# Performance work log

Hardware: AMD Instinct MI355X
Metric: run time of the kernel (lower is better)

The kernel has to match this reference:

```python
import jax, jax.numpy as jnp
import numpy as np

B, N, C, H = 8, 1024, 768, 12
D = C // H  # 64


def setup_inputs() -> dict:
    key = jax.random.key(0)
    ks = jax.random.split(key, 6)
    x = jax.random.normal(ks[0], (B, N, C), dtype=jnp.float32)
    pad_mask = jnp.ones((B, N), dtype=jnp.int32)
    # params (torch Linear stored transposed; here kept as (in, out) for x @ W)
    s = 1.0 / np.sqrt(C)
    w_attn = jax.random.uniform(ks[1], (C, 3 * C), jnp.float32, -s, s)
    b_attn = jax.random.uniform(ks[2], (3 * C,), jnp.float32, -s, s)
    w_proj = jax.random.uniform(ks[3], (C, C), jnp.float32, -s, s)
    b_proj = jax.random.uniform(ks[4], (C,), jnp.float32, -s, s)
    return {"x": x, "pad_mask": pad_mask, "w_attn": w_attn,
            "b_attn": b_attn, "w_proj": w_proj, "b_proj": b_proj}


def reference(x, pad_mask, w_attn, b_attn, w_proj, b_proj):
    # qkv projection
    qkv = x @ w_attn + b_attn                      # [B,N,3C]
    q, k, v = jnp.split(qkv, 3, axis=-1)
    q = q.reshape(B, N, H, D).transpose(0, 2, 1, 3)  # [B,H,N,D]
    k = k.reshape(B, N, H, D).transpose(0, 2, 1, 3)
    v = v.reshape(B, N, H, D).transpose(0, 2, 1, 3)
    scale = 1.0 / np.sqrt(D)
    att = jnp.einsum('bhqd,bhkd->bhqk', q, k) * scale  # [B,H,N,N]
    # NOTE: original code's causal masked_fill is non-in-place and discarded,
    # so the causal mask is NOT applied. Only the pad mask (over query rows) is.
    pm = pad_mask.reshape(B, 1, N, 1)
    att = jnp.where(pm == 0, -jnp.inf, att)
    att = jax.nn.softmax(att, axis=-1)
    out = jnp.einsum('bhqk,bhkd->bhqd', att, v)     # [B,H,N,D]
    out = out.transpose(0, 2, 1, 3).reshape(B, N, C)
    # dropout layers are identity in eval mode
    return out @ w_proj + b_proj
```

## Files before the change

### kernel.cpp

```cpp
#include <hip/hip_runtime.h>
#include <hip/hip_bf16.h>

#define B_  8
#define N_  1024
#define C_  768
#define H_  12
#define D_  64
#define C3  2304
#define C2  1536

typedef unsigned short ushort_t;
typedef __attribute__((ext_vector_type(8))) short bf16x8;
typedef __attribute__((ext_vector_type(4))) float f32x4;
typedef __attribute__((ext_vector_type(4))) unsigned int u32x4;
typedef __attribute__((ext_vector_type(2))) unsigned int u32x2;

__device__ __forceinline__ ushort_t f2bf(float f) {
    union { float f; unsigned int i; } v;
    v.f = f;
    unsigned int x = v.i;
    if ((x & 0x7f800000u) == 0x7f800000u && (x & 0x007fffffu))
        return (ushort_t)((x >> 16) | 0x0040u);
    return (ushort_t)((x + 0x7fffu + ((x >> 16) & 1u)) >> 16);
}

__device__ __forceinline__ void st1(float* p, float v) { *p = v; }
__device__ __forceinline__ void st1(ushort_t* p, float v) { *p = f2bf(v); }

#define NCVT 6144
#define NTA  1728
#define NTP  576

__device__ __forceinline__ void transpose_tile(
    const float* __restrict__ W, ushort_t* __restrict__ WT,
    int K, int Nn, int n0, int k0, float (*t)[33], int tid)
{
    const int tx = tid & 31, ty = tid >> 5;
    #pragma unroll
    for (int i = 0; i < 4; ++i) {
        const int k = ty + i * 8;
        t[k][tx] = W[(size_t)(k0 + k) * Nn + n0 + tx];
    }
    __syncthreads();
    #pragma unroll
    for (int i = 0; i < 4; ++i) {
        const int n = ty + i * 8;
        WT[(size_t)(n0 + n) * K + k0 + tx] = f2bf(t[tx][n]);
    }
}

__global__ __launch_bounds__(256) void prep(
    const float* __restrict__ X, ushort_t* __restrict__ Y,
    const float* __restrict__ Wa, ushort_t* __restrict__ WaT,
    const float* __restrict__ Wp, ushort_t* __restrict__ WpT)
{
    __shared__ float t[32][33];
    const int bid = blockIdx.x;
    const int tid = threadIdx.x;
    if (bid < NCVT) {
        const int i = (bid * 256 + tid) * 4;
        float4 f = *reinterpret_cast<const float4*>(X + i);
        ushort4 o;
        o.x = f2bf(f.x); o.y = f2bf(f.y); o.z = f2bf(f.z); o.w = f2bf(f.w);
        *reinterpret_cast<ushort4*>(Y + i) = o;
    } else if (bid < NCVT + NTA) {
        const int tt = bid - NCVT;
        transpose_tile(Wa, WaT, C_, C3, (tt % (C3 / 32)) * 32,
                       (tt / (C3 / 32)) * 32, t, tid);
    } else {
        const int tt = bid - NCVT - NTA;
        transpose_tile(Wp, WpT, C_, C_, (tt % (C_ / 32)) * 32,
                       (tt / (C_ / 32)) * 32, t, tid);
    }
}

#define GBK 64

__device__ __forceinline__ void gld_lds16(const ushort_t* g, ushort_t* lds) {
    __builtin_amdgcn_global_load_lds(
        (const __attribute__((address_space(1))) void*)g,
        (__attribute__((address_space(3))) void*)lds, 16, 0, 0);
}

template<typename TO, bool SCALEQ>
__global__ __launch_bounds__(256) void gemm_mfma(
    const ushort_t* __restrict__ A, const ushort_t* __restrict__ BT,
    const float* __restrict__ bias, TO* __restrict__ Y, int ldY,
    ushort_t* __restrict__ vtOut, int M, int K, int Nn)
{
    __shared__ ushort_t As[128 * GBK];
    __shared__ ushort_t Bs[128 * GBK];

    const int tid  = threadIdx.x;
    const int wave = tid >> 6;
    const int lane = tid & 63;

    const int nbx  = Nn / 128;
    const int nblk = nbx * (M / 128);
    const int hwid = blockIdx.y * gridDim.x + blockIdx.x;
    const int wid  = (hwid & 7) * (nblk >> 3) + (hwid >> 3);
    const int row0 = (wid / nbx) * 128;
    const int col0 = (wid % nbx) * 128;

    const int wr   = (wave >> 1) * 64;
    const int wc   = (wave & 1) * 64;
    const int l15  = lane & 15;
    const int quad = lane >> 4;
    const int l7   = l15 & 7;

    const int srow = lane >> 3;
    const int sg   = (lane & 7) ^ srow;

    f32x4 acc[4][4] = {};

    for (int k0 = 0; k0 < K; k0 += GBK) {
        __syncthreads();
        #pragma unroll
        for (int it = 0; it < 4; ++it) {
            const int baseRow = wave * 32 + it * 8;
            const int r = baseRow + srow;
            gld_lds16(&A [(size_t)(row0 + r) * K + k0 + sg * 8], &As[baseRow * GBK]);
            gld_lds16(&BT[(size_t)(col0 + r) * K + k0 + sg * 8], &Bs[baseRow * GBK]);
        }
        __syncthreads();

        #pragma unroll
        for (int kc = 0; kc < 2; ++kc) {
            bf16x8 af[4], bf[4];
            #pragma unroll
            for (int i = 0; i < 4; ++i) {
                const int aslot = (kc * 4 + quad) ^ l7;
                af[i] = *reinterpret_cast<const bf16x8*>(
                    &As[(wr + i * 16 + l15) * GBK + aslot * 8]);
                bf[i] = *reinterpret_cast<const bf16x8*>(
                    &Bs[(wc + i * 16 + l15) * GBK + aslot * 8]);
            }
            #pragma unroll
            for (int i = 0; i < 4; ++i)
                #pragma unroll
                for (int j = 0; j < 4; ++j)
                    acc[i][j] = __builtin_amdgcn_mfma_f32_16x16x32_bf16(
                        af[i], bf[j], acc[i][j], 0, 0, 0);
        }
    }

    const float qs = (SCALEQ && (col0 + wc) < C_) ? 0.1803368801f : 1.0f;

    if (vtOut != nullptr && col0 >= C2) {
        #pragma unroll
        for (int i = 0; i < 4; ++i) {
            const int r0 = row0 + wr + i * 16 + quad * 4;
            const int bb = r0 >> 10;
            const int n  = r0 & 1023;
            #pragma unroll
            for (int j = 0; j < 4; ++j) {
                const int c  = col0 + wc + j * 16 + l15;
                const int cv = c - C2;
                const int hh = cv >> 6, d = cv & 63;
                const float bv = bias[c];
                ushort4 o;
                o.x = f2bf(acc[i][j][0] + bv);
                o.y = f2bf(acc[i][j][1] + bv);
                o.z = f2bf(acc[i][j][2] + bv);
                o.w = f2bf(acc[i][j][3] + bv);
                *reinterpret_cast<ushort4*>(
                    &vtOut[((size_t)(bb * H_ + hh) * D_ + d) * N_ + n]) = o;
            }
        }
    } else {
        #pragma unroll
        for (int i = 0; i < 4; ++i) {
            const int r = row0 + wr + i * 16 + quad * 4;
            #pragma unroll
            for (int j = 0; j < 4; ++j) {
                const int c = col0 + wc + j * 16 + l15;
                const float bv = bias[c];
                #pragma unroll
                for (int t = 0; t < 4; ++t)
                    st1(&Y[(size_t)(r + t) * ldY + c], (acc[i][j][t] + bv) * qs);
            }
        }
    }
}

__global__ __launch_bounds__(256) void attn_mfma(
    const ushort_t* __restrict__ qk, const ushort_t* __restrict__ vt,
    const int* __restrict__ pad_mask, ushort_t* __restrict__ y)
{
    __shared__ __align__(16) ushort_t KV[2 * 64 * 64];
    ushort_t* const Ks  = KV;
    ushort_t* const Vts = KV + 64 * 64;

    const int tid  = threadIdx.x;
    const int wave = tid >> 6;
    const int lane = tid & 63;
    const int l15  = lane & 15;
    const int quad = lane >> 4;
    const int l7   = l15 & 7;

    const int wid = (blockIdx.x & 7) * 96 + (blockIdx.x >> 3);
    const int qt = wid & 7;
    const int hb = wid >> 3;
    const int h  = hb % H_;
    const int b  = hb / H_;
    const int q0 = qt * 128 + wave * 32;

    const ushort_t* qkB = qk + (size_t)b * N_ * C2;
    const ushort_t* vtB = vt + ((size_t)(b * H_ + h)) * D_ * N_;
    const int ho = h * D_;

    bf16x8 qf[2][2];
    #pragma unroll
    for (int rt = 0; rt < 2; ++rt)
        #pragma unroll
        for (int kc = 0; kc < 2; ++kc)
            qf[rt][kc] = *reinterpret_cast<const bf16x8*>(
                &qkB[(size_t)(q0 + rt * 16 + l15) * C2 + ho + kc * 32 + quad * 8]);

    int mrow[2][4];
    #pragma unroll
    for (int rt = 0; rt < 2; ++rt)
        #pragma unroll
        for (int t = 0; t < 4; ++t)
            mrow[rt][t] = pad_mask[b * N_ + q0 + rt * 16 + quad * 4 + t];

    f32x4 oacc[2][4] = {};
    float den[2] = {};

    const int srow = lane >> 3;
    const int sg   = (lane & 7) ^ srow;

    for (int k0 = 0; k0 < N_; k0 += 64) {
        __syncthreads();
        #pragma unroll
        for (int it = 0; it < 2; ++it) {
            const int base = wave * 16 + it * 8;
            const int r = base + srow;
            gld_lds16(&qkB[(size_t)(k0 + r) * C2 + C_ + ho + sg * 8],
                      &Ks[base * 64]);
            gld_lds16(&vtB[(size_t)r * N_ + k0 + sg * 8],
                      &Vts[base * 64]);
        }
        __syncthreads();

        f32x4 s[2][4] = {};
        #pragma unroll
        for (int kc = 0; kc < 2; ++kc) {
            bf16x8 kf[4];
            #pragma unroll
            for (int ct = 0; ct < 4; ++ct) {
                const int slot = (kc * 4 + quad) ^ l7;
                kf[ct] = *reinterpret_cast<const bf16x8*>(
                    &Ks[(ct * 16 + l15) * 64 + slot * 8]);
            }
            __builtin_amdgcn_s_setprio(1);
            #pragma unroll
            for (int rt = 0; rt < 2; ++rt)
                #pragma unroll
                for (int ct = 0; ct < 4; ++ct)
                    s[rt][ct] = __builtin_amdgcn_mfma_f32_16x16x32_bf16(
                        kf[ct], qf[rt][kc], s[rt][ct], 0, 0, 0);
            __builtin_amdgcn_s_setprio(0);
        }

        unsigned pk[2][4][2];
        #pragma unroll
        for (int rt = 0; rt < 2; ++rt)
            #pragma unroll
            for (int ct = 0; ct < 4; ++ct) {
                const unsigned x0 = __float_as_uint(
                    __builtin_amdgcn_exp2f(s[rt][ct][0])) + 0x8000u;
                const unsigned x1 = __float_as_uint(
                    __builtin_amdgcn_exp2f(s[rt][ct][1])) + 0x8000u;
                const unsigned x2 = __float_as_uint(
                    __builtin_amdgcn_exp2f(s[rt][ct][2])) + 0x8000u;
                const unsigned x3 = __float_as_uint(
                    __builtin_amdgcn_exp2f(s[rt][ct][3])) + 0x8000u;
                const unsigned c0 = (x0 >> 16) | (x1 & 0xffff0000u);
                const unsigned c1 = (x2 >> 16) | (x3 & 0xffff0000u);
                den[rt] += __uint_as_float(c0 << 16)
                         + __uint_as_float(c0 & 0xffff0000u)
                         + __uint_as_float(c1 << 16)
                         + __uint_as_float(c1 & 0xffff0000u);
                pk[rt][ct][0] = c0;
                pk[rt][ct][1] = c1;
            }

        #pragma unroll
        for (int kc = 0; kc < 2; ++kc) {
            bf16x8 pf[2], vf[4];
            #pragma unroll
            for (int rt = 0; rt < 2; ++rt) {
                const u32x4 pw = (u32x4){pk[rt][kc * 2][0], pk[rt][kc * 2][1],
                                         pk[rt][kc * 2 + 1][0],
                                         pk[rt][kc * 2 + 1][1]};
                pf[rt] = __builtin_bit_cast(bf16x8, pw);
            }
            #pragma unroll
            for (int dt = 0; dt < 4; ++dt) {
                const int d  = dt * 16 + l15;
                const int g1 = kc * 4 + (quad >> 1);
                const int o  = (quad & 1) * 4;
                const u32x2 va = *reinterpret_cast<const u32x2*>(
                    &Vts[d * 64 + ((g1 ^ l7)) * 8 + o]);
                const u32x2 vb = *reinterpret_cast<const u32x2*>(
                    &Vts[d * 64 + (((g1 + 2) ^ l7)) * 8 + o]);
                const u32x4 wv = __builtin_shufflevector(va, vb, 0, 1, 2, 3);
                vf[dt] = __builtin_bit_cast(bf16x8, wv);
            }
            __builtin_amdgcn_s_setprio(1);
            #pragma unroll
            for (int rt = 0; rt < 2; ++rt)
                #pragma unroll
                for (int dt = 0; dt < 4; ++dt)
                    oacc[rt][dt] = __builtin_amdgcn_mfma_f32_16x16x32_bf16(
                        pf[rt], vf[dt], oacc[rt][dt], 0, 0, 0);
            __builtin_amdgcn_s_setprio(0);
        }
    }

    __syncthreads();
    ushort_t* const scratch = KV + wave * 32 * 64;

    #pragma unroll
    for (int rt = 0; rt < 2; ++rt) {
        float v = den[rt];
        v += __shfl_xor(v, 16);
        v += __shfl_xor(v, 32);
        den[rt] = v;
    }
    #pragma unroll
    for (int rt = 0; rt < 2; ++rt)
        #pragma unroll
        for (int t = 0; t < 4; ++t) {
            const float dv  = __shfl(den[rt], quad * 4 + t);
            const float inv = mrow[rt][t] ? 1.0f / dv : __builtin_nanf("");
            const int row = rt * 16 + quad * 4 + t;
            #pragma unroll
            for (int dt = 0; dt < 4; ++dt) {
                const int slot = (dt * 2 + (l15 >> 3)) ^ (row & 7);
                scratch[row * 64 + slot * 8 + l7] =
                    f2bf(oacc[rt][dt][t] * inv);
            }
        }
    __syncthreads();
    {
        const int orow = lane >> 1;
        const int og   = (lane & 1) * 4;
        const size_t gr = (size_t)(b * N_ + q0 + orow) * C_ + ho;
        #pragma unroll
        for (int i2 = 0; i2 < 4; ++i2) {
            const int g = og + i2;
            uint4 w = *reinterpret_cast<const uint4*>(
                &scratch[orow * 64 + (g ^ (orow & 7)) * 8]);
            *reinterpret_cast<uint4*>(&y[gr + g * 8]) = w;
        }
    }
}

extern "C" void kernel_launch(void* const* d_in, const int* in_sizes, int n_in,
                              void* d_out, int out_size, void* d_ws, size_t ws_size,
                              hipStream_t stream)
{
    const float* x      = (const float*)d_in[0];
    const int*   pad    = (const int*)d_in[1];
    const float* w_attn = (const float*)d_in[2];
    const float* b_attn = (const float*)d_in[3];
    const float* w_proj = (const float*)d_in[4];
    const float* b_proj = (const float*)d_in[5];
    float* out = (float*)d_out;

    ushort_t* qkb = (ushort_t*)d_ws;
    ushort_t* vtb = qkb + (size_t)B_ * N_ * C2;
    ushort_t* y   = vtb + (size_t)B_ * H_ * D_ * N_;
    ushort_t* xb  = y;
    ushort_t* wat = y + (size_t)B_ * N_ * C_;
    ushort_t* wpt = wat + (size_t)C3 * C_;

    const int M = B_ * N_;

    prep<<<dim3(NCVT + NTA + NTP), dim3(256), 0, stream>>>(
        x, xb, w_attn, wat, w_proj, wpt);

    gemm_mfma<ushort_t, true><<<dim3(C3 / 128, M / 128), dim3(256), 0, stream>>>(
        xb, wat, b_attn, qkb, C2, vtb, M, C_, C3);

    attn_mfma<<<dim3(B_ * H_ * 8), dim3(256), 0, stream>>>(qkb, vtb, pad, y);

    gemm_mfma<float, false><<<dim3(C_ / 128, M / 128), dim3(256), 0, stream>>>(
        y, wpt, b_proj, out, C_, nullptr, M, C_, C_);
}
```

Baseline: 192.9 us.

## Double-buffer LDS tiles in GEMM and attention, permute V^T layout for 128-bit loads

Both the GEMM and attention kernels now use two LDS buffers and prefetch the next K/V or A/B tile while computing on the current one, with a single barrier per iteration. This is meant to hide global-to-LDS load latency. The V-transpose writer permutes the sequence index so the attention kernel can read V fragments with one 16-byte LDS load instead of two 8-byte loads plus a shuffle. The softmax denominator is now summed from the unrounded fp32 exponentials rather than the bf16-rounded values. The cost is doubled LDS per block, which may reduce occupancy.

```diff
diff --git a/kernel.cpp b/kernel.cpp
--- a/kernel.cpp
+++ b/kernel.cpp
@@ -13,7 +13,6 @@
 typedef __attribute__((ext_vector_type(8))) short bf16x8;
 typedef __attribute__((ext_vector_type(4))) float f32x4;
 typedef __attribute__((ext_vector_type(4))) unsigned int u32x4;
-typedef __attribute__((ext_vector_type(2))) unsigned int u32x2;
 
 __device__ __forceinline__ ushort_t f2bf(float f) {
     union { float f; unsigned int i; } v;
@@ -88,8 +87,7 @@
     const float* __restrict__ bias, TO* __restrict__ Y, int ldY,
     ushort_t* __restrict__ vtOut, int M, int K, int Nn)
 {
-    __shared__ ushort_t As[128 * GBK];
-    __shared__ ushort_t Bs[128 * GBK];
+    __shared__ ushort_t AB[2][2 * 128 * GBK];
 
     const int tid  = threadIdx.x;
     const int wave = tid >> 6;
@@ -113,16 +111,34 @@
 
     f32x4 acc[4][4] = {};
 
-    for (int k0 = 0; k0 < K; k0 += GBK) {
-        __syncthreads();
-        #pragma unroll
-        for (int it = 0; it < 4; ++it) {
-            const int baseRow = wave * 32 + it * 8;
-            const int r = baseRow + srow;
-            gld_lds16(&A [(size_t)(row0 + r) * K + k0 + sg * 8], &As[baseRow * GBK]);
-            gld_lds16(&BT[(size_t)(col0 + r) * K + k0 + sg * 8], &Bs[baseRow * GBK]);
-        }
-        __syncthreads();
+    #pragma unroll
+    for (int it = 0; it < 4; ++it) {
+        const int baseRow = wave * 32 + it * 8;
+        const int r = baseRow + srow;
+        gld_lds16(&A [(size_t)(row0 + r) * K + sg * 8], &AB[0][baseRow * GBK]);
+        gld_lds16(&BT[(size_t)(col0 + r) * K + sg * 8],
+                  &AB[0][128 * GBK + baseRow * GBK]);
+    }
+    __syncthreads();
+
+    const int nsteps = K / GBK;
+    for (int t = 0; t < nsteps; ++t) {
+        const int buf = t & 1;
+        const ushort_t* const As = AB[buf];
+        const ushort_t* const Bs = AB[buf] + 128 * GBK;
+
+        if (t + 1 < nsteps) {
+            const int k0 = (t + 1) * GBK;
+            #pragma unroll
+            for (int it = 0; it < 4; ++it) {
+                const int baseRow = wave * 32 + it * 8;
+                const int r = baseRow + srow;
+                gld_lds16(&A [(size_t)(row0 + r) * K + k0 + sg * 8],
+                          &AB[buf ^ 1][baseRow * GBK]);
+                gld_lds16(&BT[(size_t)(col0 + r) * K + k0 + sg * 8],
+                          &AB[buf ^ 1][128 * GBK + baseRow * GBK]);
+            }
+        }
 
         #pragma unroll
         for (int kc = 0; kc < 2; ++kc) {
@@ -142,6 +158,7 @@
                     acc[i][j] = __builtin_amdgcn_mfma_f32_16x16x32_bf16(
                         af[i], bf[j], acc[i][j], 0, 0, 0);
         }
+        __syncthreads();
     }
 
     const float qs = (SCALEQ && (col0 + wc) < C_) ? 0.1803368801f : 1.0f;
@@ -152,6 +169,7 @@
             const int r0 = row0 + wr + i * 16 + quad * 4;
             const int bb = r0 >> 10;
             const int n  = r0 & 1023;
+            const int np = (n & 0x3E0) | (quad << 3) | ((i & 1) << 2);
             #pragma unroll
             for (int j = 0; j < 4; ++j) {
                 const int c  = col0 + wc + j * 16 + l15;
@@ -164,7 +182,7 @@
                 o.z = f2bf(acc[i][j][2] + bv);
                 o.w = f2bf(acc[i][j][3] + bv);
                 *reinterpret_cast<ushort4*>(
-                    &vtOut[((size_t)(bb * H_ + hh) * D_ + d) * N_ + n]) = o;
+                    &vtOut[((size_t)(bb * H_ + hh) * D_ + d) * N_ + np]) = o;
             }
         }
     } else {
@@ -187,9 +205,7 @@
     const ushort_t* __restrict__ qk, const ushort_t* __restrict__ vt,
     const int* __restrict__ pad_mask, ushort_t* __restrict__ y)
 {
-    __shared__ __align__(16) ushort_t KV[2 * 64 * 64];
-    ushort_t* const Ks  = KV;
-    ushort_t* const Vts = KV + 64 * 64;
+    __shared__ __align__(16) ushort_t KV[2][2 * 64 * 64];
 
     const int tid  = threadIdx.x;
     const int wave = tid >> 6;
@@ -230,18 +246,32 @@
     const int srow = lane >> 3;
     const int sg   = (lane & 7) ^ srow;
 
-    for (int k0 = 0; k0 < N_; k0 += 64) {
-        __syncthreads();
-        #pragma unroll
-        for (int it = 0; it < 2; ++it) {
-            const int base = wave * 16 + it * 8;
-            const int r = base + srow;
-            gld_lds16(&qkB[(size_t)(k0 + r) * C2 + C_ + ho + sg * 8],
-                      &Ks[base * 64]);
-            gld_lds16(&vtB[(size_t)r * N_ + k0 + sg * 8],
-                      &Vts[base * 64]);
-        }
-        __syncthreads();
+    #pragma unroll
+    for (int it = 0; it < 2; ++it) {
+        const int base = wave * 16 + it * 8;
+        const int r = base + srow;
+        gld_lds16(&qkB[(size_t)r * C2 + C_ + ho + sg * 8], &KV[0][base * 64]);
+        gld_lds16(&vtB[(size_t)r * N_ + sg * 8], &KV[0][4096 + base * 64]);
+    }
+    __syncthreads();
+
+    for (int t = 0; t < N_ / 64; ++t) {
+        const int buf = t & 1;
+        const ushort_t* const Ks  = KV[buf];
+        const ushort_t* const Vts = KV[buf] + 4096;
+
+        if (t + 1 < N_ / 64) {
+            const int k0 = (t + 1) * 64;
+            #pragma unroll
+            for (int it = 0; it < 2; ++it) {
+                const int base = wave * 16 + it * 8;
+                const int r = base + srow;
+                gld_lds16(&qkB[(size_t)(k0 + r) * C2 + C_ + ho + sg * 8],
+                          &KV[buf ^ 1][base * 64]);
+                gld_lds16(&vtB[(size_t)r * N_ + k0 + sg * 8],
+                          &KV[buf ^ 1][4096 + base * 64]);
+            }
+        }
 
         f32x4 s[2][4] = {};
         #pragma unroll
@@ -268,22 +298,17 @@
         for (int rt = 0; rt < 2; ++rt)
             #pragma unroll
             for (int ct = 0; ct < 4; ++ct) {
-                const unsigned x0 = __float_as_uint(
-                    __builtin_amdgcn_exp2f(s[rt][ct][0])) + 0x8000u;
-                const unsigned x1 = __float_as_uint(
-                    __builtin_amdgcn_exp2f(s[rt][ct][1])) + 0x8000u;
-                const unsigned x2 = __float_as_uint(
-                    __builtin_amdgcn_exp2f(s[rt][ct][2])) + 0x8000u;
-                const unsigned x3 = __float_as_uint(
-                    __builtin_amdgcn_exp2f(s[rt][ct][3])) + 0x8000u;
-                const unsigned c0 = (x0 >> 16) | (x1 & 0xffff0000u);
-                const unsigned c1 = (x2 >> 16) | (x3 & 0xffff0000u);
-                den[rt] += __uint_as_float(c0 << 16)
-                         + __uint_as_float(c0 & 0xffff0000u)
-                         + __uint_as_float(c1 << 16)
-                         + __uint_as_float(c1 & 0xffff0000u);
-                pk[rt][ct][0] = c0;
-                pk[rt][ct][1] = c1;
+                const float p0 = __builtin_amdgcn_exp2f(s[rt][ct][0]);
+                const float p1 = __builtin_amdgcn_exp2f(s[rt][ct][1]);
+                const float p2 = __builtin_amdgcn_exp2f(s[rt][ct][2]);
+                const float p3 = __builtin_amdgcn_exp2f(s[rt][ct][3]);
+                den[rt] += (p0 + p1) + (p2 + p3);
+                const unsigned x0 = __float_as_uint(p0) + 0x8000u;
+                const unsigned x1 = __float_as_uint(p1) + 0x8000u;
+                const unsigned x2 = __float_as_uint(p2) + 0x8000u;
+                const unsigned x3 = __float_as_uint(p3) + 0x8000u;
+                pk[rt][ct][0] = (x0 >> 16) | (x1 & 0xffff0000u);
+                pk[rt][ct][1] = (x2 >> 16) | (x3 & 0xffff0000u);
             }
 
         #pragma unroll
@@ -298,15 +323,9 @@
             }
             #pragma unroll
             for (int dt = 0; dt < 4; ++dt) {
-                const int d  = dt * 16 + l15;
-                const int g1 = kc * 4 + (quad >> 1);
-                const int o  = (quad & 1) * 4;
-                const u32x2 va = *reinterpret_cast<const u32x2*>(
-                    &Vts[d * 64 + ((g1 ^ l7)) * 8 + o]);
-                const u32x2 vb = *reinterpret_cast<const u32x2*>(
-                    &Vts[d * 64 + (((g1 + 2) ^ l7)) * 8 + o]);
-                const u32x4 wv = __builtin_shufflevector(va, vb, 0, 1, 2, 3);
-                vf[dt] = __builtin_bit_cast(bf16x8, wv);
+                const int slot = (kc * 4 + quad) ^ l7;
+                vf[dt] = *reinterpret_cast<const bf16x8*>(
+                    &Vts[(dt * 16 + l15) * 64 + slot * 8]);
             }
             __builtin_amdgcn_s_setprio(1);
             #pragma unroll
@@ -317,10 +336,10 @@
                         pf[rt], vf[dt], oacc[rt][dt], 0, 0, 0);
             __builtin_amdgcn_s_setprio(0);
         }
-    }
-
-    __syncthreads();
-    ushort_t* const scratch = KV + wave * 32 * 64;
+        __syncthreads();
+    }
+
+    ushort_t* const scratch = KV[0] + wave * 32 * 64;
 
     #pragma unroll
     for (int rt = 0; rt < 2; ++rt) {
```

After: 193.6 us, median of 2. About the same (+0.4%).
